# Kernel tuning notes

Hardware: AMD Instinct MI355X
Metric: run time of the kernel (lower is better)

Reference implementation:

```python
import jax, jax.numpy as jnp
import numpy as np

B, S, H = 16, 512, 384
NUM_BINS = 256  # torch.clamp(mean, 0, 255) embedding bins


def setup_inputs() -> dict:
    key = jax.random.key(0)
    k1, k2, k3, k4, k5, k6 = jax.random.split(key, 6)
    encoder_output = jax.random.normal(k1, (B, S, H), dtype=jnp.float32)
    # log-durations in [0, 2) -> durations round(exp(d)-1) in {0..6}
    log_duration = jax.random.uniform(k2, (B, S), dtype=jnp.float32) * 2.0
    pitch = jax.random.uniform(k3, (B, S), dtype=jnp.float32) * 255.0
    energy = jax.random.uniform(k4, (B, S), dtype=jnp.float32) * 255.0
    pitch_emb_table = jax.random.normal(k5, (NUM_BINS, H), dtype=jnp.float32)
    energy_emb_table = jax.random.normal(k6, (NUM_BINS, H), dtype=jnp.float32)
    return {
        "encoder_output": encoder_output,
        "log_duration": log_duration,
        "pitch": pitch,
        "energy": energy,
        "pitch_emb_table": pitch_emb_table,
        "energy_emb_table": energy_emb_table,
        "max_mel_len": 2000,
    }


def reference(encoder_output, log_duration, pitch, energy,
              pitch_emb_table, energy_emb_table, max_mel_len):
    # duration = clamp(round(exp(log_d) - 1), min=0).long()
    duration = jnp.maximum(jnp.round(jnp.exp(log_duration) - 1.0), 0.0).astype(jnp.int32)  # [B,S]

    # LengthRegulatorTRT: interval mask via cumsum, then mask-multiply-sum
    cum = jnp.cumsum(duration, axis=1)                       # [B,S] end offsets
    total_len = cum[:, -1]                                   # [B]
    start = jnp.concatenate([jnp.zeros((duration.shape[0], 1), jnp.int32), cum[:, :-1]], axis=1)
    positions = jnp.arange(max_mel_len, dtype=jnp.int32)     # [L]
    mask = (positions[None, None, :] >= start[:, :, None]) & \
           (positions[None, None, :] < cum[:, :, None])      # [B,S,L]
    # identical math to (x[:,:,None,:] * mask[...,None]).sum(1), but fused
    output = jnp.einsum('bsh,bsl->blh', encoder_output,
                        mask.astype(encoder_output.dtype))    # [B,L,H]
    mel_len = jnp.minimum(total_len, max_mel_len).astype(jnp.int32)  # [B]

    # pitch/energy mean -> long -> clamp(0,255) -> embedding, broadcast-add
    pitch_idx = jnp.clip(jnp.mean(pitch, axis=1, keepdims=True).astype(jnp.int32), 0, NUM_BINS - 1)   # [B,1]
    energy_idx = jnp.clip(jnp.mean(energy, axis=1, keepdims=True).astype(jnp.int32), 0, NUM_BINS - 1)  # [B,1]
    output = output + pitch_emb_table[pitch_idx]   # [B,1,H] broadcasts over L
    output = output + energy_emb_table[energy_idx]
    return output, mel_len
```

## Files before the change

kernel.cpp:

```cpp
#include <hip/hip_runtime.h>

#define BB 16
#define SS 512
#define HH 384
#define LL 2000
#define NBINS 256
#define H4 (HH/4)
#define OUT0 (BB*LL*HH)

__global__ __launch_bounds__(512) void prep_kernel(
    const float* __restrict__ log_dur,
    const float* __restrict__ pitch,
    const float* __restrict__ energy,
    const float* __restrict__ ptab,
    const float* __restrict__ etab,
    int*   __restrict__ pos_map,
    float* __restrict__ comb,
    float* __restrict__ out_mel)
{
    const int b = blockIdx.x;
    const int t = threadIdx.x;

    __shared__ int   cum[SS];
    __shared__ float red[SS];
    __shared__ int   s_idx[2];
    __shared__ int   s_total;

    float ld = log_dur[b*SS + t];
    float e  = expf(ld) - 1.0f;
    int   d  = (int)fmaxf(rintf(e), 0.0f);

    cum[t] = d;
    __syncthreads();
    for (int off = 1; off < SS; off <<= 1) {
        int v = (t >= off) ? cum[t - off] : 0;
        __syncthreads();
        cum[t] += v;
        __syncthreads();
    }

    red[t] = pitch[b*SS + t];
    __syncthreads();
    for (int off = SS/2; off > 0; off >>= 1) {
        if (t < off) red[t] += red[t + off];
        __syncthreads();
    }
    if (t == 0) {
        int idx = (int)(red[0] * (1.0f/SS));
        s_idx[0] = idx < 0 ? 0 : (idx > NBINS-1 ? NBINS-1 : idx);
    }
    __syncthreads();

    red[t] = energy[b*SS + t];
    __syncthreads();
    for (int off = SS/2; off > 0; off >>= 1) {
        if (t < off) red[t] += red[t + off];
        __syncthreads();
    }
    if (t == 0) {
        int idx = (int)(red[0] * (1.0f/SS));
        s_idx[1] = idx < 0 ? 0 : (idx > NBINS-1 ? NBINS-1 : idx);
        s_total  = cum[SS-1];
        int mel  = s_total < LL ? s_total : LL;
        out_mel[b] = (float)mel;
    }
    __syncthreads();

    const int pidx  = s_idx[0];
    const int eidx  = s_idx[1];
    const int total = s_total;

    if (t < HH) comb[b*HH + t] = ptab[pidx*HH + t] + etab[eidx*HH + t];

    for (int l = t; l < LL; l += SS) {
        int sm = -1;
        if (l < total) {
            int lo = 0, hi = SS - 1;
            while (lo < hi) {
                int mid = (lo + hi) >> 1;
                if (cum[mid] > l) hi = mid; else lo = mid + 1;
            }
            sm = lo;
        }
        pos_map[b*LL + l] = sm;
    }
}

__global__ __launch_bounds__(256) void expand_kernel(
    const float4* __restrict__ enc,
    const int*    __restrict__ pos_map,
    const float4* __restrict__ comb,
    float4*       __restrict__ out)
{
    const int i = blockIdx.x * 256 + threadIdx.x;
    if (i >= BB*LL*H4) return;
    const int h4  = i % H4;
    const int row = i / H4;
    const int b   = row / LL;
    const int s   = pos_map[row];

    float4 c = comb[b*H4 + h4];
    float4 v = c;
    if (s >= 0) {
        float4 a = enc[(b*SS + s)*H4 + h4];
        v.x = a.x + c.x; v.y = a.y + c.y; v.z = a.z + c.z; v.w = a.w + c.w;
    }
    out[i] = v;
}

extern "C" void kernel_launch(void* const* d_in, const int* in_sizes, int n_in,
                              void* d_out, int out_size, void* d_ws, size_t ws_size,
                              hipStream_t stream) {
    const float* enc      = (const float*)d_in[0];
    const float* log_dur  = (const float*)d_in[1];
    const float* pitch    = (const float*)d_in[2];
    const float* energy   = (const float*)d_in[3];
    const float* ptab     = (const float*)d_in[4];
    const float* etab     = (const float*)d_in[5];

    float* out = (float*)d_out;

    int*   pos_map = (int*)d_ws;
    float* comb    = (float*)((char*)d_ws + BB*LL*sizeof(int));

    prep_kernel<<<BB, SS, 0, stream>>>(log_dur, pitch, energy, ptab, etab,
                                       pos_map, comb, out + OUT0);

    const int n4 = BB*LL*H4;
    expand_kernel<<<(n4 + 255)/256, 256, 0, stream>>>(
        (const float4*)enc, pos_map, (const float4*)comb, (float4*)out);
}
```

Measured before the change: 95.79 us.

## Fuse prep and expand into one kernel with per-block redundant scan

Merges the prefix-sum/reduction prep kernel and the expand kernel into a single launch. Each of 75 blocks per batch row recomputes the duration scan, the pitch/energy means and the combined embedding in shared memory, then writes its slice of the output. Each output element now runs a binary search directly instead of reading a precomputed position map. This removes a launch, the global pos_map round trip and the serialization between kernels. In exchange it repeats the scan in every block and performs one binary search per float4 rather than one per row, and only 1200 blocks are launched.

New measurement: 95.17 us. About the same (-0.6%).

```diff
diff --git a/kernel.cpp b/kernel.cpp
--- a/kernel.cpp
+++ b/kernel.cpp
@@ -7,126 +7,122 @@
 #define NBINS 256
 #define H4 (HH/4)
 #define OUT0 (BB*LL*HH)
+#define BLOCKS_PER_B 75
+#define CHUNK ((LL*H4)/BLOCKS_PER_B)
 
-__global__ __launch_bounds__(512) void prep_kernel(
-    const float* __restrict__ log_dur,
-    const float* __restrict__ pitch,
-    const float* __restrict__ energy,
-    const float* __restrict__ ptab,
-    const float* __restrict__ etab,
-    int*   __restrict__ pos_map,
-    float* __restrict__ comb,
-    float* __restrict__ out_mel)
+__global__ __launch_bounds__(256) void fused_kernel(
+    const float4* __restrict__ enc,
+    const float*  __restrict__ log_dur,
+    const float*  __restrict__ pitch,
+    const float*  __restrict__ energy,
+    const float4* __restrict__ ptab,
+    const float4* __restrict__ etab,
+    float4*       __restrict__ out,
+    float*        __restrict__ out_mel)
 {
-    const int b = blockIdx.x;
-    const int t = threadIdx.x;
+    const int b     = blockIdx.x / BLOCKS_PER_B;
+    const int chunk = blockIdx.x % BLOCKS_PER_B;
+    const int t     = threadIdx.x;
 
-    __shared__ int   cum[SS];
-    __shared__ float red[SS];
-    __shared__ int   s_idx[2];
-    __shared__ int   s_total;
+    __shared__ int    sa[SS], sb[SS];
+    __shared__ float  red[256];
+    __shared__ float4 comb4[H4];
+    __shared__ int    s_pidx, s_eidx, s_total;
 
-    float ld = log_dur[b*SS + t];
-    float e  = expf(ld) - 1.0f;
-    int   d  = (int)fmaxf(rintf(e), 0.0f);
+    {
+        float ld0 = log_dur[b*SS + t];
+        float ld1 = log_dur[b*SS + t + 256];
+        sa[t]     = (int)fmaxf(rintf(expf(ld0) - 1.0f), 0.0f);
+        sa[t+256] = (int)fmaxf(rintf(expf(ld1) - 1.0f), 0.0f);
+    }
+    __syncthreads();
 
-    cum[t] = d;
+    int* src = sa; int* dst = sb;
+    for (int off = 1; off < SS; off <<= 1) {
+        for (int i = t; i < SS; i += 256) {
+            int v = src[i];
+            if (i >= off) v += src[i - off];
+            dst[i] = v;
+        }
+        __syncthreads();
+        int* tmp = src; src = dst; dst = tmp;
+    }
+    const int* cum = src;
+
+    red[t] = pitch[b*SS + t] + pitch[b*SS + t + 256];
     __syncthreads();
-    for (int off = 1; off < SS; off <<= 1) {
-        int v = (t >= off) ? cum[t - off] : 0;
-        __syncthreads();
-        cum[t] += v;
-        __syncthreads();
-    }
-
-    red[t] = pitch[b*SS + t];
-    __syncthreads();
-    for (int off = SS/2; off > 0; off >>= 1) {
+    for (int off = 128; off > 0; off >>= 1) {
         if (t < off) red[t] += red[t + off];
         __syncthreads();
     }
     if (t == 0) {
         int idx = (int)(red[0] * (1.0f/SS));
-        s_idx[0] = idx < 0 ? 0 : (idx > NBINS-1 ? NBINS-1 : idx);
+        s_pidx = idx < 0 ? 0 : (idx > NBINS-1 ? NBINS-1 : idx);
     }
     __syncthreads();
 
-    red[t] = energy[b*SS + t];
+    red[t] = energy[b*SS + t] + energy[b*SS + t + 256];
     __syncthreads();
-    for (int off = SS/2; off > 0; off >>= 1) {
+    for (int off = 128; off > 0; off >>= 1) {
         if (t < off) red[t] += red[t + off];
         __syncthreads();
     }
     if (t == 0) {
         int idx = (int)(red[0] * (1.0f/SS));
-        s_idx[1] = idx < 0 ? 0 : (idx > NBINS-1 ? NBINS-1 : idx);
-        s_total  = cum[SS-1];
-        int mel  = s_total < LL ? s_total : LL;
-        out_mel[b] = (float)mel;
+        s_eidx  = idx < 0 ? 0 : (idx > NBINS-1 ? NBINS-1 : idx);
+        s_total = cum[SS-1];
+        if (chunk == 0) {
+            int mel = s_total < LL ? s_total : LL;
+            out_mel[b] = (float)mel;
+        }
     }
     __syncthreads();
 
-    const int pidx  = s_idx[0];
-    const int eidx  = s_idx[1];
+    if (t < H4) {
+        float4 p = ptab[s_pidx*H4 + t];
+        float4 q = etab[s_eidx*H4 + t];
+        comb4[t] = make_float4(p.x+q.x, p.y+q.y, p.z+q.z, p.w+q.w);
+    }
+    __syncthreads();
+
     const int total = s_total;
+    const int base  = chunk * CHUNK;
+    const int out_b = b * (LL*H4);
 
-    if (t < HH) comb[b*HH + t] = ptab[pidx*HH + t] + etab[eidx*HH + t];
-
-    for (int l = t; l < LL; l += SS) {
-        int sm = -1;
+    #pragma unroll 2
+    for (int k = 0; k < CHUNK; k += 256) {
+        int idx = base + k + t;
+        int h4  = idx % H4;
+        int l   = idx / H4;
+        float4 v = comb4[h4];
         if (l < total) {
             int lo = 0, hi = SS - 1;
             while (lo < hi) {
                 int mid = (lo + hi) >> 1;
                 if (cum[mid] > l) hi = mid; else lo = mid + 1;
             }
-            sm = lo;
+            float4 a = enc[(b*SS + lo)*H4 + h4];
+            v.x += a.x; v.y += a.y; v.z += a.z; v.w += a.w;
         }
-        pos_map[b*LL + l] = sm;
+        out[out_b + idx] = v;
     }
-}
-
-__global__ __launch_bounds__(256) void expand_kernel(
-    const float4* __restrict__ enc,
-    const int*    __restrict__ pos_map,
-    const float4* __restrict__ comb,
-    float4*       __restrict__ out)
-{
-    const int i = blockIdx.x * 256 + threadIdx.x;
-    if (i >= BB*LL*H4) return;
-    const int h4  = i % H4;
-    const int row = i / H4;
-    const int b   = row / LL;
-    const int s   = pos_map[row];
-
-    float4 c = comb[b*H4 + h4];
-    float4 v = c;
-    if (s >= 0) {
-        float4 a = enc[(b*SS + s)*H4 + h4];
-        v.x = a.x + c.x; v.y = a.y + c.y; v.z = a.z + c.z; v.w = a.w + c.w;
-    }
-    out[i] = v;
 }
 
 extern "C" void kernel_launch(void* const* d_in, const int* in_sizes, int n_in,
                               void* d_out, int out_size, void* d_ws, size_t ws_size,
                               hipStream_t stream) {
-    const float* enc      = (const float*)d_in[0];
-    const float* log_dur  = (const float*)d_in[1];
-    const float* pitch    = (const float*)d_in[2];
-    const float* energy   = (const float*)d_in[3];
-    const float* ptab     = (const float*)d_in[4];
-    const float* etab     = (const float*)d_in[5];
+    const float* enc     = (const float*)d_in[0];
+    const float* log_dur = (const float*)d_in[1];
+    const float* pitch   = (const float*)d_in[2];
+    const float* energy  = (const float*)d_in[3];
+    const float* ptab    = (const float*)d_in[4];
+    const float* etab    = (const float*)d_in[5];
+    (void)d_ws; (void)ws_size;
 
     float* out = (float*)d_out;
 
-    int*   pos_map = (int*)d_ws;
-    float* comb    = (float*)((char*)d_ws + BB*LL*sizeof(int));
-
-    prep_kernel<<<BB, SS, 0, stream>>>(log_dur, pitch, energy, ptab, etab,
-                                       pos_map, comb, out + OUT0);
-
-    const int n4 = BB*LL*H4;
-    expand_kernel<<<(n4 + 255)/256, 256, 0, stream>>>(
-        (const float4*)enc, pos_map, (const float4*)comb, (float4*)out);
+    fused_kernel<<<BB*BLOCKS_PER_B, 256, 0, stream>>>(
+        (const float4*)enc, log_dur, pitch, energy,
+        (const float4*)ptab, (const float4*)etab,
+        (float4*)out, out + OUT0);
 }
```
